# Kernel tuning notes

Measured on AMD Instinct MI355X. Metric: run time of the kernel, lower is better.

The kernel has to match this reference:

```python
import jax, jax.numpy as jnp
import numpy as np
import math

B, T, D, H = 4, 1024, 1024, 16
HD = D // H  # 64
ROPE_BASE = 10000.0


def _apply_rope(q, k):
    # q, k: [B, H, T, HD]; interleaved even/odd rotation as in RotaryEmbedding
    t_len = q.shape[2]
    half = q.shape[-1] // 2
    inv_freq = 1.0 / (ROPE_BASE ** (jnp.arange(half, dtype=jnp.float32) / half))
    freqs = jnp.arange(t_len, dtype=jnp.float32)[:, None] * inv_freq  # [T, half]
    cos = jnp.cos(freqs)
    sin = jnp.sin(freqs)

    def rot(u):
        u1 = u[..., ::2]   # even lanes
        u2 = u[..., 1::2]  # odd lanes
        e = u1 * cos - u2 * sin
        o = u2 * cos + u1 * sin
        return jnp.stack([e, o], axis=-1).reshape(u.shape)

    return rot(q), rot(k)


def _split_heads(x):
    b, t, d = x.shape
    return x.reshape(b, t, H, HD).transpose(0, 2, 1, 3)  # [B,H,T,HD]


def _mha(x, Wq, bq, Wk, bk, Wv, bv, Wo, bo, mask):
    q = _split_heads(jnp.einsum('btd,ed->bte', x, Wq) + bq)
    k = _split_heads(jnp.einsum('btd,ed->bte', x, Wk) + bk)
    v = _split_heads(jnp.einsum('btd,ed->bte', x, Wv) + bv)
    q, k = _apply_rope(q, k)
    scores = jnp.einsum('bhtd,bhsd->bhts', q.astype(jnp.float32),
                        k.astype(jnp.float32)) / math.sqrt(HD)
    scores = jnp.where(mask, scores, -jnp.inf)
    attn = jax.nn.softmax(scores, axis=-1).astype(v.dtype)
    ctx = jnp.einsum('bhts,bhsd->bhtd', attn.astype(jnp.float32),
                     v.astype(jnp.float32)).astype(v.dtype)
    ctx = ctx.transpose(0, 2, 1, 3).reshape(x.shape[0], x.shape[1], D)
    z = jnp.einsum('btd,ed->bte', ctx, Wo) + bo
    return z


def setup_inputs() -> dict:
    key = jax.random.key(0)
    ks = jax.random.split(key, 9)
    s = 0.02
    inp = {
        'x':  jax.random.normal(ks[0], (B, T, D), jnp.float32),
        'Wq': jax.random.normal(ks[1], (D, D), jnp.float32) * s,
        'bq': jax.random.normal(ks[2], (D,), jnp.float32) * s,
        'Wk': jax.random.normal(ks[3], (D, D), jnp.float32) * s,
        'bk': jax.random.normal(ks[4], (D,), jnp.float32) * s,
        'Wv': jax.random.normal(ks[5], (D, D), jnp.float32) * s,
        'bv': jax.random.normal(ks[6], (D,), jnp.float32) * s,
        'Wo': jax.random.normal(ks[7], (D, D), jnp.float32) * s,
        'bo': jax.random.normal(ks[8], (D,), jnp.float32) * s,
        'mask': jnp.tril(jnp.ones((T, T), dtype=bool))[None, None],  # causal
    }
    return inp


def reference(x, Wq, bq, Wk, bk, Wv, bv, Wo, bo, mask):
    return _mha(x, Wq, bq, Wk, bk, Wv, bv, Wo, bo, mask)
```

## Files before the change

### kernel.cpp

```cpp
#include <hip/hip_runtime.h>


#define T_SEQ 1024
#define NH    16
#define HDIM  64
#define DM    1024
#define MTOK  4096

typedef __attribute__((ext_vector_type(8))) short short8;
typedef __attribute__((ext_vector_type(4))) float f32x4;
typedef unsigned short u16;

__device__ __forceinline__ u16 f2bf(float f) {
  unsigned int u = __builtin_bit_cast(unsigned int, f);
  u += 0x7fffu + ((u >> 16) & 1u);
  return (u16)(u >> 16);
}

__device__ __forceinline__ void gll16(const void* g, void* l) {
  __builtin_amdgcn_global_load_lds(
      (const __attribute__((address_space(1))) unsigned int*)(unsigned long long)(g),
      (__attribute__((address_space(3))) unsigned int*)(unsigned int)(unsigned long long)(l),
      16, 0, 0);
}

__global__ void prep_kernel(const float* __restrict__ x,
                            const float* __restrict__ Wq, const float* __restrict__ Wk,
                            const float* __restrict__ Wv, const float* __restrict__ Wo,
                            u16* __restrict__ xb, u16* __restrict__ wall,
                            float* __restrict__ ctab, float* __restrict__ stab) {
  const int bid = blockIdx.x, tid = threadIdx.x;
  if (bid < 8192) {
    const float* src;
    u16* dst;
    int i;
    if (bid < 4096) {
      src = x; dst = xb; i = bid * 256 + tid;
    } else {
      const int w = (bid - 4096) >> 10;
      src = w == 0 ? Wq : w == 1 ? Wk : w == 2 ? Wv : Wo;
      dst = wall + (size_t)w * (DM * DM);
      i = ((bid - 4096) & 1023) * 256 + tid;
    }
    float4 f = ((const float4*)src)[i];
    unsigned long long pk = (unsigned long long)f2bf(f.x)
                          | ((unsigned long long)f2bf(f.y) << 16)
                          | ((unsigned long long)f2bf(f.z) << 32)
                          | ((unsigned long long)f2bf(f.w) << 48);
    ((unsigned long long*)dst)[i] = pk;
  } else {
    const int idx = (bid - 8192) * 256 + tid;
    const int t = idx >> 5, i = idx & 31;
    float inv = powf(10000.f, -(float)i * (1.0f / 32.0f));
    float f = (float)t * inv;
    ctab[idx] = cosf(f);
    stab[idx] = sinf(f);
  }
}

__device__ __forceinline__ void gemm_pipe(
    const u16* __restrict__ A, const u16* __restrict__ Bw,
    int m0, int n0, u16* As, u16* Bs, f32x4 acc[4][4]) {
  const int tid = threadIdx.x, lane = tid & 63, wave = tid >> 6;
  const int wr = wave >> 1, wc = wave & 1;
  const int swz = ((tid & 3) ^ ((tid >> 3) & 3)) * 8;
  const size_t Aofs = (size_t)(m0 + (tid >> 2)) * DM + swz;
  const size_t Bofs = (size_t)(n0 + (tid >> 2)) * DM + swz;
  const int ldst = tid * 8;
  const int NT = DM / 32;

#define STAGE_T(t, b)                                                   \
  do {                                                                  \
    gll16(&A[Aofs + (t) * 32],         &As[(b) * 4096 + ldst]);         \
    gll16(&A[Aofs + 65536 + (t) * 32], &As[(b) * 4096 + 2048 + ldst]);  \
    gll16(&Bw[Bofs + (t) * 32],        &Bs[(b) * 4096 + ldst]);         \
    gll16(&Bw[Bofs + 65536 + (t) * 32], &Bs[(b) * 4096 + 2048 + ldst]); \
  } while (0)

  STAGE_T(0, 0);
  STAGE_T(1, 1);
  const int arow = (wr * 64 + (lane & 15)) * 32 + (((lane >> 4) ^ ((lane >> 1) & 3)) * 8);
  const int brow = (wc * 64 + (lane & 15)) * 32 + (((lane >> 4) ^ ((lane >> 1) & 3)) * 8);
  int cbuf = 0, sbuf = 2;
  for (int t = 0; t < NT; ++t) {
    if (t + 1 < NT) {
      asm volatile("s_waitcnt vmcnt(4)" ::: "memory");
    } else {
      asm volatile("s_waitcnt vmcnt(0)" ::: "memory");
    }
    asm volatile("s_barrier" ::: "memory");
    if (t + 2 < NT) STAGE_T(t + 2, sbuf);
    short8 af[4], bf[4];
#pragma unroll
    for (int i = 0; i < 4; ++i) {
      af[i] = *(const short8*)&As[cbuf * 4096 + arow + i * 512];
      bf[i] = *(const short8*)&Bs[cbuf * 4096 + brow + i * 512];
    }
#pragma unroll
    for (int i = 0; i < 4; ++i)
#pragma unroll
      for (int j = 0; j < 4; ++j)
        acc[i][j] = __builtin_amdgcn_mfma_f32_16x16x32_bf16(af[i], bf[j], acc[i][j], 0, 0, 0);
    asm volatile("s_waitcnt lgkmcnt(0)" ::: "memory");
    asm volatile("s_barrier" ::: "memory");
    cbuf = cbuf == 2 ? 0 : cbuf + 1;
    sbuf = sbuf == 2 ? 0 : sbuf + 1;
  }
#undef STAGE_T
}

__global__ __launch_bounds__(256) void qkv_kernel(
    const u16* __restrict__ xb, const u16* __restrict__ wqkv,
    const float* __restrict__ bq, const float* __restrict__ bk, const float* __restrict__ bv,
    const float* __restrict__ ctab, const float* __restrict__ stab,
    u16* __restrict__ qbuf, u16* __restrict__ kbuf, u16* __restrict__ vt) {
  __shared__ __align__(16) u16 As[3 * 4096];
  __shared__ __align__(16) u16 Bs[3 * 4096];
  const int m0 = blockIdx.y * 128;
  const int n0 = blockIdx.x * 128;
  const int mode = n0 >> 10;
  const float* bias = mode == 0 ? bq : (mode == 1 ? bk : bv);
  f32x4 acc[4][4];
#pragma unroll
  for (int i = 0; i < 4; ++i)
#pragma unroll
    for (int j = 0; j < 4; ++j)
#pragma unroll
      for (int r = 0; r < 4; ++r) acc[i][j][r] = 0.f;
  gemm_pipe(xb, wqkv, m0, n0, As, Bs, acc);

  const int lane = threadIdx.x & 63, wave = threadIdx.x >> 6;
  const int wr = wave >> 1, wc = wave & 1;
#pragma unroll
  for (int i = 0; i < 4; ++i) {
#pragma unroll
    for (int j = 0; j < 4; ++j) {
      const int e = n0 + wc * 64 + j * 16 + (lane & 15);
      const float bval = bias[e & 1023];
      const int h = (e >> 6) & 15, hd = e & 63;
#pragma unroll
      for (int r = 0; r < 4; ++r) {
        const int m = m0 + wr * 64 + i * 16 + ((lane >> 4) * 4) + r;
        const int b = m >> 10, t = m & 1023;
        float v = acc[i][j][r] + bval;
        if (mode < 2) {
          float p = __shfl_xor(v, 1);
          const int fi = hd >> 1;
          const float cc = ctab[t * 32 + fi], ss = stab[t * 32 + fi];
          v = (hd & 1) ? (v * cc + p * ss) : (v * cc - p * ss);
          u16* dst = mode == 0 ? qbuf : kbuf;
          dst[(((size_t)(b * NH + h) * T_SEQ + t) << 6) + hd] = f2bf(v);
        } else {
          vt[(((size_t)(b * NH + h) * HDIM + hd) << 10) + t] = f2bf(v);
        }
      }
    }
  }
}

__global__ __launch_bounds__(256) void attn_kernel(
    const u16* __restrict__ qbuf, const u16* __restrict__ kbuf,
    const u16* __restrict__ vtb, u16* __restrict__ ctx) {
  __shared__ __align__(16) u16 Ks[2][64 * 64];
  __shared__ __align__(16) u16 Vs[2][64 * 64];
  __shared__ __align__(16) u16 Psm[4][16 * 64];
  const int bh = blockIdx.x;
  const int b = bh >> 4, h = bh & 15;
  const int tid = threadIdx.x, lane = tid & 63, wave = tid >> 6;
  const u16* Qp = qbuf + (size_t)bh * T_SEQ * HDIM;
  const u16* Kp = kbuf + (size_t)bh * T_SEQ * HDIM;
  const u16* Vp = vtb + (size_t)bh * HDIM * T_SEQ;
  u16* Pw = &Psm[wave][0];

  const int srow = tid >> 3;
  const int schx = ((tid & 7) ^ (srow & 7)) * 8;
  const int lx = lane & 7;

#define STG(kvt, bb)                                                            \
  do {                                                                          \
    _Pragma("unroll") for (int c = 0; c < 2; ++c) {                             \
      const int rr = c * 32 + srow;                                             \
      gll16(&Kp[(kvt) * 4096 + rr * 64 + schx], &Ks[bb][c * 2048 + tid * 8]);   \
      gll16(&Vp[(size_t)rr * T_SEQ + (kvt) * 64 + schx], &Vs[bb][c * 2048 + tid * 8]); \
    }                                                                           \
  } while (0)

  for (int phase = 0; phase < 2; ++phase) {
    const int qt = phase ? (15 - (int)blockIdx.y) : (int)blockIdx.y;
    const int q0 = qt * 64;
    const int nkv = qt + 1;
    const int qrow = q0 + wave * 16 + (lane & 15);
    const short8 qf0 = *(const short8*)&Qp[qrow * 64 + ((lane >> 4) * 8)];
    const short8 qf1 = *(const short8*)&Qp[qrow * 64 + 32 + ((lane >> 4) * 8)];

    f32x4 acc_o[4];
    float m_r[4], l_r[4];
#pragma unroll
    for (int i = 0; i < 4; ++i) {
#pragma unroll
      for (int r = 0; r < 4; ++r) acc_o[i][r] = 0.f;
      m_r[i] = -__builtin_inff();
      l_r[i] = 0.f;
    }

    __syncthreads();
    STG(0, 0);
    int cur = 0;

    for (int kvt = 0; kvt < nkv; ++kvt) {
      __syncthreads();
      if (kvt + 1 < nkv) STG(kvt + 1, cur ^ 1);

      f32x4 sacc[4];
#pragma unroll
      for (int cb = 0; cb < 4; ++cb) {
#pragma unroll
        for (int r = 0; r < 4; ++r) sacc[cb][r] = 0.f;
        const int krow = cb * 16 + (lane & 15);
        const short8 kf0 = *(const short8*)&Ks[cur][krow * 64 + (((lane >> 4) ^ lx) * 8)];
        const short8 kf1 = *(const short8*)&Ks[cur][krow * 64 + (((4 + (lane >> 4)) ^ lx) * 8)];
        sacc[cb] = __builtin_amdgcn_mfma_f32_16x16x32_bf16(qf0, kf0, sacc[cb], 0, 0, 0);
        sacc[cb] = __builtin_amdgcn_mfma_f32_16x16x32_bf16(qf1, kf1, sacc[cb], 0, 0, 0);
      }
      const int trow_base = q0 + wave * 16 + ((lane >> 4) * 4);
#pragma unroll
      for (int cb = 0; cb < 4; ++cb) {
        const int scol = kvt * 64 + cb * 16 + (lane & 15);
#pragma unroll
        for (int r = 0; r < 4; ++r) {
          float sv = sacc[cb][r] * 0.125f;
          sacc[cb][r] = (scol > trow_base + r) ? -__builtin_inff() : sv;
        }
      }
      float mt[4];
#pragma unroll
      for (int r = 0; r < 4; ++r)
        mt[r] = fmaxf(fmaxf(sacc[0][r], sacc[1][r]), fmaxf(sacc[2][r], sacc[3][r]));
#pragma unroll
      for (int off = 1; off < 16; off <<= 1)
#pragma unroll
        for (int r = 0; r < 4; ++r) mt[r] = fmaxf(mt[r], __shfl_xor(mt[r], off));
      float sf[4], lt[4];
#pragma unroll
      for (int r = 0; r < 4; ++r) {
        const float mn = fmaxf(m_r[r], mt[r]);
        sf[r] = __expf(m_r[r] - mn);
        m_r[r] = mn;
        lt[r] = 0.f;
      }
#pragma unroll
      for (int cb = 0; cb < 4; ++cb)
#pragma unroll
        for (int r = 0; r < 4; ++r) {
          const float p = __expf(sacc[cb][r] - m_r[r]);
          sacc[cb][r] = p;
          lt[r] += p;
        }
#pragma unroll
      for (int off = 1; off < 16; off <<= 1)
#pragma unroll
        for (int r = 0; r < 4; ++r) lt[r] += __shfl_xor(lt[r], off);
#pragma unroll
      for (int r = 0; r < 4; ++r) l_r[r] = l_r[r] * sf[r] + lt[r];
#pragma unroll
      for (int hb = 0; hb < 4; ++hb)
#pragma unroll
        for (int r = 0; r < 4; ++r) acc_o[hb][r] *= sf[r];

#pragma unroll
      for (int cb = 0; cb < 4; ++cb)
#pragma unroll
        for (int r = 0; r < 4; ++r) {
          const int prow = (lane >> 4) * 4 + r;
          Pw[prow * 64 + ((cb * 16 + (lane & 15)) ^ ((prow & 7) << 3))] = f2bf(sacc[cb][r]);
        }

      const int prr = lane & 15;
#pragma unroll
      for (int kc = 0; kc < 2; ++kc) {
        const short8 pf = *(const short8*)&Pw[prr * 64 + (((kc * 4 + (lane >> 4)) ^ lx) * 8)];
#pragma unroll
        for (int hb = 0; hb < 4; ++hb) {
          const int vrow = hb * 16 + (lane & 15);
          const short8 vf = *(const short8*)&Vs[cur][vrow * 64 + (((kc * 4 + (lane >> 4)) ^ lx) * 8)];
          acc_o[hb] = __builtin_amdgcn_mfma_f32_16x16x32_bf16(pf, vf, acc_o[hb], 0, 0, 0);
        }
      }
      cur ^= 1;
    }

#pragma unroll
    for (int hb = 0; hb < 4; ++hb) {
      const int hd = hb * 16 + (lane & 15);
#pragma unroll
      for (int r = 0; r < 4; ++r) {
        const int t = q0 + wave * 16 + ((lane >> 4) * 4) + r;
        const float v = acc_o[hb][r] / l_r[r];
        ctx[((size_t)(b * T_SEQ + t) * NH + h) * HDIM + hd] = f2bf(v);
      }
    }
  }
#undef STG
}

__global__ __launch_bounds__(256) void oproj_kernel(
    const u16* __restrict__ ctx, const u16* __restrict__ Wob,
    const float* __restrict__ bo, float* __restrict__ out) {
  __shared__ __align__(16) u16 As[3 * 4096];
  __shared__ __align__(16) u16 Bs[3 * 4096];
  const int m0 = blockIdx.y * 128, n0 = blockIdx.x * 128;
  f32x4 acc[4][4];
#pragma unroll
  for (int i = 0; i < 4; ++i)
#pragma unroll
    for (int j = 0; j < 4; ++j)
#pragma unroll
      for (int r = 0; r < 4; ++r) acc[i][j][r] = 0.f;
  gemm_pipe(ctx, Wob, m0, n0, As, Bs, acc);
  const int lane = threadIdx.x & 63, wave = threadIdx.x >> 6;
  const int wr = wave >> 1, wc = wave & 1;
#pragma unroll
  for (int i = 0; i < 4; ++i)
#pragma unroll
    for (int j = 0; j < 4; ++j) {
      const int e = n0 + wc * 64 + j * 16 + (lane & 15);
      const float bval = bo[e];
#pragma unroll
      for (int r = 0; r < 4; ++r) {
        const int m = m0 + wr * 64 + i * 16 + ((lane >> 4) * 4) + r;
        out[(size_t)m * DM + e] = acc[i][j][r] + bval;
      }
    }
}

extern "C" void kernel_launch(void* const* d_in, const int* in_sizes, int n_in,
                              void* d_out, int out_size, void* d_ws, size_t ws_size,
                              hipStream_t stream) {
  const float* x  = (const float*)d_in[0];
  const float* Wq = (const float*)d_in[1];
  const float* bq = (const float*)d_in[2];
  const float* Wk = (const float*)d_in[3];
  const float* bk = (const float*)d_in[4];
  const float* Wv = (const float*)d_in[5];
  const float* bv = (const float*)d_in[6];
  const float* Wo = (const float*)d_in[7];
  const float* bo = (const float*)d_in[8];

  char* w = (char*)d_ws;
  u16* xb   = (u16*)(w);
  u16* wall = (u16*)(w + (8ull << 20));
  u16* wob  = (u16*)(w + (14ull << 20));
  u16* qb   = (u16*)(w + (16ull << 20));
  u16* kb   = (u16*)(w + (24ull << 20));
  u16* vtb  = (u16*)(w + (32ull << 20));
  u16* ctxb = (u16*)(w + (40ull << 20));
  float* ctab = (float*)(w + (48ull << 20));
  float* stab = ctab + T_SEQ * 32;

  prep_kernel<<<dim3(8192 + 128), 256, 0, stream>>>(x, Wq, Wk, Wv, Wo, xb, wall, ctab, stab);
  qkv_kernel<<<dim3(3 * DM / 128, MTOK / 128), 256, 0, stream>>>(
      xb, wall, bq, bk, bv, ctab, stab, qb, kb, vtb);
  attn_kernel<<<dim3(64, 8), 256, 0, stream>>>(qb, kb, vtb, ctxb);
  oproj_kernel<<<dim3(DM / 128, MTOK / 128), 256, 0, stream>>>(ctxb, wob, bo, (float*)d_out);
}
```

Before: 116.1 us.

## Retile QKV and output-projection GEMMs with K=64 double-buffered pipeline

Replaces the triple-buffered K=32 GEMM pipeline with a templated double-buffered K=64 pipeline that uses an XOR-swizzled LDS layout and __syncthreads. The QKV GEMM moves to 128x192 tiles, giving 16x32 blocks and computing the bias mode per column. The output projection moves to 64x128 tiles to double its block count. Both kernels request 2 blocks per CU via launch bounds. The aim is to raise MFMA work per barrier and improve occupancy and wave balance on the GPU. In exchange, only one K tile is prefetched ahead, and the larger tiles add register pressure.

```diff
diff --git a/kernel.cpp b/kernel.cpp
--- a/kernel.cpp
+++ b/kernel.cpp
@@ -58,84 +58,91 @@
   }
 }
 
-__device__ __forceinline__ void gemm_pipe(
+template<int BM, int BN, int AI, int BI, int MI, int NJ>
+__device__ __forceinline__ void gemm_pipe2(
     const u16* __restrict__ A, const u16* __restrict__ Bw,
-    int m0, int n0, u16* As, u16* Bs, f32x4 acc[4][4]) {
+    int m0, int n0, u16* As, u16* Bs, f32x4 acc[MI][NJ]) {
   const int tid = threadIdx.x, lane = tid & 63, wave = tid >> 6;
   const int wr = wave >> 1, wc = wave & 1;
-  const int swz = ((tid & 3) ^ ((tid >> 3) & 3)) * 8;
-  const size_t Aofs = (size_t)(m0 + (tid >> 2)) * DM + swz;
-  const size_t Bofs = (size_t)(n0 + (tid >> 2)) * DM + swz;
-  const int ldst = tid * 8;
-  const int NT = DM / 32;
-
-#define STAGE_T(t, b)                                                   \
-  do {                                                                  \
-    gll16(&A[Aofs + (t) * 32],         &As[(b) * 4096 + ldst]);         \
-    gll16(&A[Aofs + 65536 + (t) * 32], &As[(b) * 4096 + 2048 + ldst]);  \
-    gll16(&Bw[Bofs + (t) * 32],        &Bs[(b) * 4096 + ldst]);         \
-    gll16(&Bw[Bofs + 65536 + (t) * 32], &Bs[(b) * 4096 + 2048 + ldst]); \
+  const int srcswz = ((lane & 7) ^ (lane >> 3)) * 8;
+  const int NT = DM / 64;
+
+#define STAGE2(t, b)                                                         \
+  do {                                                                       \
+    _Pragma("unroll") for (int i = 0; i < AI; ++i) {                         \
+      const int q = (wave * AI + i) * 64 + lane;                             \
+      gll16(&A[(size_t)(m0 + (q >> 3)) * DM + (t) * 64 + srcswz],            \
+            &As[(b) * BM * 64 + q * 8]);                                     \
+    }                                                                        \
+    _Pragma("unroll") for (int i = 0; i < BI; ++i) {                         \
+      const int q = (wave * BI + i) * 64 + lane;                             \
+      gll16(&Bw[(size_t)(n0 + (q >> 3)) * DM + (t) * 64 + srcswz],           \
+            &Bs[(b) * BN * 64 + q * 8]);                                     \
+    }                                                                        \
   } while (0)
 
-  STAGE_T(0, 0);
-  STAGE_T(1, 1);
-  const int arow = (wr * 64 + (lane & 15)) * 32 + (((lane >> 4) ^ ((lane >> 1) & 3)) * 8);
-  const int brow = (wc * 64 + (lane & 15)) * 32 + (((lane >> 4) ^ ((lane >> 1) & 3)) * 8);
-  int cbuf = 0, sbuf = 2;
+  STAGE2(0, 0);
+  __syncthreads();
+  int buf = 0;
+  const int arow0 = wr * (BM / 2) + (lane & 15);
+  const int brow0 = wc * (BN / 2) + (lane & 15);
+  const int c0 = (((lane >> 4)) ^ (lane & 7)) * 8;
+  const int c1 = ((4 + (lane >> 4)) ^ (lane & 7)) * 8;
   for (int t = 0; t < NT; ++t) {
-    if (t + 1 < NT) {
-      asm volatile("s_waitcnt vmcnt(4)" ::: "memory");
-    } else {
-      asm volatile("s_waitcnt vmcnt(0)" ::: "memory");
-    }
-    asm volatile("s_barrier" ::: "memory");
-    if (t + 2 < NT) STAGE_T(t + 2, sbuf);
-    short8 af[4], bf[4];
-#pragma unroll
-    for (int i = 0; i < 4; ++i) {
-      af[i] = *(const short8*)&As[cbuf * 4096 + arow + i * 512];
-      bf[i] = *(const short8*)&Bs[cbuf * 4096 + brow + i * 512];
-    }
-#pragma unroll
-    for (int i = 0; i < 4; ++i)
-#pragma unroll
-      for (int j = 0; j < 4; ++j)
-        acc[i][j] = __builtin_amdgcn_mfma_f32_16x16x32_bf16(af[i], bf[j], acc[i][j], 0, 0, 0);
-    asm volatile("s_waitcnt lgkmcnt(0)" ::: "memory");
-    asm volatile("s_barrier" ::: "memory");
-    cbuf = cbuf == 2 ? 0 : cbuf + 1;
-    sbuf = sbuf == 2 ? 0 : sbuf + 1;
+    if (t + 1 < NT) STAGE2(t + 1, buf ^ 1);
+    short8 af[MI][2], bf[NJ][2];
+#pragma unroll
+    for (int i = 0; i < MI; ++i) {
+      const int r = buf * BM * 64 + (arow0 + i * 16) * 64;
+      af[i][0] = *(const short8*)&As[r + c0];
+      af[i][1] = *(const short8*)&As[r + c1];
+    }
+#pragma unroll
+    for (int j = 0; j < NJ; ++j) {
+      const int r = buf * BN * 64 + (brow0 + j * 16) * 64;
+      bf[j][0] = *(const short8*)&Bs[r + c0];
+      bf[j][1] = *(const short8*)&Bs[r + c1];
+    }
+#pragma unroll
+    for (int i = 0; i < MI; ++i)
+#pragma unroll
+      for (int j = 0; j < NJ; ++j) {
+        acc[i][j] = __builtin_amdgcn_mfma_f32_16x16x32_bf16(af[i][0], bf[j][0], acc[i][j], 0, 0, 0);
+        acc[i][j] = __builtin_amdgcn_mfma_f32_16x16x32_bf16(af[i][1], bf[j][1], acc[i][j], 0, 0, 0);
+      }
+    __syncthreads();
+    buf ^= 1;
   }
-#undef STAGE_T
-}
-
-__global__ __launch_bounds__(256) void qkv_kernel(
+#undef STAGE2
+}
+
+__global__ __launch_bounds__(256, 2) void qkv_kernel(
     const u16* __restrict__ xb, const u16* __restrict__ wqkv,
     const float* __restrict__ bq, const float* __restrict__ bk, const float* __restrict__ bv,
     const float* __restrict__ ctab, const float* __restrict__ stab,
     u16* __restrict__ qbuf, u16* __restrict__ kbuf, u16* __restrict__ vt) {
-  __shared__ __align__(16) u16 As[3 * 4096];
-  __shared__ __align__(16) u16 Bs[3 * 4096];
+  __shared__ __align__(16) u16 As[2 * 128 * 64];
+  __shared__ __align__(16) u16 Bs[2 * 192 * 64];
   const int m0 = blockIdx.y * 128;
-  const int n0 = blockIdx.x * 128;
-  const int mode = n0 >> 10;
-  const float* bias = mode == 0 ? bq : (mode == 1 ? bk : bv);
-  f32x4 acc[4][4];
+  const int n0 = blockIdx.x * 192;
+  f32x4 acc[4][6];
 #pragma unroll
   for (int i = 0; i < 4; ++i)
 #pragma unroll
-    for (int j = 0; j < 4; ++j)
+    for (int j = 0; j < 6; ++j)
 #pragma unroll
       for (int r = 0; r < 4; ++r) acc[i][j][r] = 0.f;
-  gemm_pipe(xb, wqkv, m0, n0, As, Bs, acc);
+  gemm_pipe2<128, 192, 4, 6, 4, 6>(xb, wqkv, m0, n0, As, Bs, acc);
 
   const int lane = threadIdx.x & 63, wave = threadIdx.x >> 6;
   const int wr = wave >> 1, wc = wave & 1;
 #pragma unroll
   for (int i = 0; i < 4; ++i) {
 #pragma unroll
-    for (int j = 0; j < 4; ++j) {
-      const int e = n0 + wc * 64 + j * 16 + (lane & 15);
+    for (int j = 0; j < 6; ++j) {
+      const int e = n0 + wc * 96 + j * 16 + (lane & 15);
+      const int mode = e >> 10;
+      const float* bias = mode == 0 ? bq : (mode == 1 ? bk : bv);
       const float bval = bias[e & 1023];
       const int h = (e >> 6) & 15, hd = e & 63;
 #pragma unroll
@@ -303,31 +310,31 @@
 #undef STG
 }
 
-__global__ __launch_bounds__(256) void oproj_kernel(
+__global__ __launch_bounds__(256, 2) void oproj_kernel(
     const u16* __restrict__ ctx, const u16* __restrict__ Wob,
     const float* __restrict__ bo, float* __restrict__ out) {
-  __shared__ __align__(16) u16 As[3 * 4096];
-  __shared__ __align__(16) u16 Bs[3 * 4096];
-  const int m0 = blockIdx.y * 128, n0 = blockIdx.x * 128;
-  f32x4 acc[4][4];
-#pragma unroll
-  for (int i = 0; i < 4; ++i)
+  __shared__ __align__(16) u16 As[2 * 64 * 64];
+  __shared__ __align__(16) u16 Bs[2 * 128 * 64];
+  const int m0 = blockIdx.y * 64, n0 = blockIdx.x * 128;
+  f32x4 acc[2][4];
+#pragma unroll
+  for (int i = 0; i < 2; ++i)
 #pragma unroll
     for (int j = 0; j < 4; ++j)
 #pragma unroll
       for (int r = 0; r < 4; ++r) acc[i][j][r] = 0.f;
-  gemm_pipe(ctx, Wob, m0, n0, As, Bs, acc);
+  gemm_pipe2<64, 128, 2, 4, 2, 4>(ctx, Wob, m0, n0, As, Bs, acc);
   const int lane = threadIdx.x & 63, wave = threadIdx.x >> 6;
   const int wr = wave >> 1, wc = wave & 1;
 #pragma unroll
-  for (int i = 0; i < 4; ++i)
+  for (int i = 0; i < 2; ++i)
 #pragma unroll
     for (int j = 0; j < 4; ++j) {
       const int e = n0 + wc * 64 + j * 16 + (lane & 15);
       const float bval = bo[e];
 #pragma unroll
       for (int r = 0; r < 4; ++r) {
-        const int m = m0 + wr * 64 + i * 16 + ((lane >> 4) * 4) + r;
+        const int m = m0 + wr * 32 + i * 16 + ((lane >> 4) * 4) + r;
         out[(size_t)m * DM + e] = acc[i][j][r] + bval;
       }
     }
@@ -358,8 +365,8 @@
   float* stab = ctab + T_SEQ * 32;
 
   prep_kernel<<<dim3(8192 + 128), 256, 0, stream>>>(x, Wq, Wk, Wv, Wo, xb, wall, ctab, stab);
-  qkv_kernel<<<dim3(3 * DM / 128, MTOK / 128), 256, 0, stream>>>(
+  qkv_kernel<<<dim3(3 * DM / 192, MTOK / 128), 256, 0, stream>>>(
       xb, wall, bq, bk, bv, ctab, stab, qb, kb, vtb);
   attn_kernel<<<dim3(64, 8), 256, 0, stream>>>(qb, kb, vtb, ctxb);
-  oproj_kernel<<<dim3(DM / 128, MTOK / 128), 256, 0, stream>>>(ctxb, wob, bo, (float*)d_out);
-}
+  oproj_kernel<<<dim3(DM / 128, MTOK / 64), 256, 0, stream>>>(ctxb, wob, bo, (float*)d_out);
+}
```

Result: faster. 109.9 us (-5.3%).
